# Kernel tuning notes

Hardware: AMD Instinct MI355X
Metric: run time of the kernel (lower is better)

Reference implementation:

```python
import jax, jax.numpy as jnp
import numpy as np

N, DIM = 100000, 512
HID = DIM // 2


def _mlp(z, W1, b1, W2, b2):
    # shared scorer: [N, dim] -> [N, 1]
    h = jax.nn.relu(z @ W1 + b1)
    return h @ W2 + b2


def setup_inputs() -> dict:
    key = jax.random.key(0)
    k1, k2, k3, k4 = jax.random.split(key, 4)
    s1 = 1.0 / np.sqrt(DIM)
    s2 = 1.0 / np.sqrt(HID)
    return {
        "z1": jax.random.normal(k1, (N, DIM), dtype=jnp.float32),
        "z2": jax.random.normal(k2, (N, DIM), dtype=jnp.float32),
        "W1": jax.random.normal(k3, (DIM, HID), dtype=jnp.float32) * s1,
        "b1": jnp.zeros((HID,), dtype=jnp.float32),
        "W2": jax.random.normal(k4, (HID, 1), dtype=jnp.float32) * s2,
        "b2": jnp.zeros((1,), dtype=jnp.float32),
    }


def reference(z1, z2, W1, b1, W2, b2):
    x = _mlp(z1, W1, b1, W2, b2)  # [N, 1]
    y = _mlp(z2, W1, b1, W2, b2)  # [N, 1]
    # exp-normalize pair: score_x = e^x / (e^x + e^y) == sigmoid(x - y)
    # computed exactly as in the original (plain exp, no max-subtract)
    e_x = jnp.exp(x)
    e_y = jnp.exp(y)
    denom = e_x + e_y
    score_x = e_x / denom  # [N, 1]
    score_y = e_y / denom  # [N, 1]
    # diag(score) @ z  ==  score * z  (row-wise broadcast scale)
    return score_x * z1 + score_y * z2
```

## Files before the change

kernel.cpp:

```cpp
#include <hip/hip_runtime.h>
#include <hip/hip_bf16.h>
#include <cmath>

#define DIM 512
#define HID 256
#define ROWS_PB 32
#define NCHUNK 16
#define CB 16384

typedef __attribute__((ext_vector_type(8))) short short8;
typedef __attribute__((ext_vector_type(4))) float f32x4;
typedef __attribute__((ext_vector_type(4))) unsigned int u32x4;

__device__ __forceinline__ unsigned short f2bf(float f) {
  union { float f; unsigned u; } v; v.f = f;
  unsigned u = v.u;
  return (unsigned short)((u + 0x7FFFu + ((u >> 16) & 1u)) >> 16);
}
__device__ __forceinline__ float bf2f(short h) {
  union { unsigned u; float f; } v;
  v.u = ((unsigned)(unsigned short)h) << 16;
  return v.f;
}

#define LGKM_BAR()                                        \
  do {                                                    \
    asm volatile("s_waitcnt lgkmcnt(0)" ::: "memory");    \
    __builtin_amdgcn_s_barrier();                         \
    __builtin_amdgcn_sched_barrier(0);                    \
  } while (0)

__global__ void w1_swz_kernel(const float* __restrict__ W1,
                              unsigned short* __restrict__ w1s) {
  int tid = blockIdx.x * blockDim.x + threadIdx.x;
  if (tid >= DIM * HID) return;
  int k = tid / HID;
  int c = tid - k * HID;
  w1s[(((k >> 3) * HID) + c) * 8 + (k & 7)] = f2bf(W1[tid]);
}

__device__ __forceinline__ short8 cvt8(const f32x4 p0, const f32x4 p1) {
  short8 r;
  r[0] = (short)f2bf(p0[0]); r[1] = (short)f2bf(p0[1]);
  r[2] = (short)f2bf(p0[2]); r[3] = (short)f2bf(p0[3]);
  r[4] = (short)f2bf(p1[0]); r[5] = (short)f2bf(p1[1]);
  r[6] = (short)f2bf(p1[2]); r[7] = (short)f2bf(p1[3]);
  return r;
}

__device__ __forceinline__ void wcombine(float wa, const short8 a, float wb,
                                         const short8 b, f32x4& o0, f32x4& o1) {
#pragma unroll
  for (int i = 0; i < 4; ++i) {
    o0[i] = wa * bf2f(a[i]) + wb * bf2f(b[i]);
    o1[i] = wa * bf2f(a[i + 4]) + wb * bf2f(b[i + 4]);
  }
}

__global__ __launch_bounds__(256, 2) void fa_main_kernel(
    const float* __restrict__ z1, const float* __restrict__ z2,
    const unsigned short* __restrict__ w1s,
    const float* __restrict__ bias1, const float* __restrict__ W2,
    const float* __restrict__ bias2, float* __restrict__ out, int n) {
  __shared__ char smem[81920];
  short8* Az = (short8*)smem;
  char* Bs = smem + 65536;
  float* xs = (float*)(smem + 65536);

  const int t = threadIdx.x;
  const int w = t >> 6;
  const int l = t & 63;
  const int l15 = l & 15, l16 = l >> 4;
  const int s = w & 1;
  const int tl = w >> 1;
  const int row0 = blockIdx.x * ROWS_PB;
  const int myrow = row0 + tl * 16 + l15;
  const bool rok = myrow < n;
  const float* zz = s ? z2 : z1;
  const float* ap = zz + (size_t)myrow * DIM + (l16 << 3);
  const f32x4 zf4 = (f32x4){0.f, 0.f, 0.f, 0.f};

  u32x4 breg0, breg1, breg2, breg3;
#define BLOAD(c)                                            \
  {                                                         \
    const u32x4* g = (const u32x4*)w1s + (c) * 1024 + t;    \
    breg0 = g[0];                                           \
    breg1 = g[256];                                         \
    breg2 = g[512];                                         \
    breg3 = g[768];                                         \
  }
#define BWRITE()                                            \
  {                                                         \
    u32x4* d = (u32x4*)Bs + t;                              \
    d[0] = breg0;                                           \
    d[256] = breg1;                                         \
    d[512] = breg2;                                         \
    d[768] = breg3;                                         \
  }

  BLOAD(0);
  f32x4 paA0, paA1, paB0, paB1;
  paA0 = rok ? *(const f32x4*)(ap) : zf4;
  paA1 = rok ? *(const f32x4*)(ap + 4) : zf4;
  paB0 = rok ? *(const f32x4*)(ap + 32) : zf4;
  paB1 = rok ? *(const f32x4*)(ap + 36) : zf4;
  BWRITE();
  __syncthreads();

  f32x4 acc[16];
#pragma unroll
  for (int f = 0; f < 16; ++f) acc[f] = zf4;

#pragma unroll
  for (int c = 0; c < NCHUNK; ++c) {
    if (c + 1 < NCHUNK) BLOAD(c + 1);
    short8 af;
    if (c & 1)
      af = cvt8(paB0, paB1);
    else
      af = cvt8(paA0, paA1);
    Az[((s * NCHUNK + c) * 2 + tl) * 64 + l] = af;
    if (c + 2 < NCHUNK) {
      const float* apn = ap + ((c + 2) << 5);
      if (c & 1) {
        paB0 = rok ? *(const f32x4*)(apn) : zf4;
        paB1 = rok ? *(const f32x4*)(apn + 4) : zf4;
      } else {
        paA0 = rok ? *(const f32x4*)(apn) : zf4;
        paA1 = rok ? *(const f32x4*)(apn + 4) : zf4;
      }
    }
    __builtin_amdgcn_sched_barrier(0);
    const short8* bp = (const short8*)Bs + (l16 << 8) + l15;
    short8 bf[16];
#pragma unroll
    for (int f = 0; f < 16; ++f) bf[f] = bp[f << 4];
    __builtin_amdgcn_sched_barrier(0);
#pragma unroll
    for (int f = 0; f < 16; ++f)
      acc[f] =
          __builtin_amdgcn_mfma_f32_16x16x32_bf16(af, bf[f], acc[f], 0, 0, 0);
    LGKM_BAR();
    if (c + 1 < NCHUNK) BWRITE();
    LGKM_BAR();
  }

  float part[4] = {0.f, 0.f, 0.f, 0.f};
#pragma unroll
  for (int f = 0; f < 16; ++f) {
    const int cc = (f << 4) + l15;
    const float w2v = W2[cc];
    const float b1v = bias1[cc];
#pragma unroll
    for (int r = 0; r < 4; ++r) {
      const float hh = acc[f][r] + b1v;
      part[r] += (hh > 0.f) ? hh * w2v : 0.f;
    }
  }
#pragma unroll
  for (int r = 0; r < 4; ++r) {
#pragma unroll
    for (int m = 1; m < 16; m <<= 1) part[r] += __shfl_xor(part[r], m, 16);
  }
  if (l15 == 0) {
#pragma unroll
    for (int r = 0; r < 4; ++r)
      xs[s * ROWS_PB + tl * 16 + (l16 << 2) + r] = part[r];
  }
  __syncthreads();

  const float x = xs[tl * 16 + l15];
  const float y = xs[ROWS_PB + tl * 16 + l15];
  const float sx = 1.f / (1.f + __expf(y - x));
  const float sy = 1.f - sx;
  float* orow = out + (size_t)myrow * DIM + (l16 << 3);
  if (rok) {
#pragma unroll
    for (int j = 0; j < 8; ++j) {
      const int cc = (s << 3) + j;
      const short8 a0 = Az[((0 * NCHUNK + cc) * 2 + tl) * 64 + l];
      const short8 a1 = Az[((1 * NCHUNK + cc) * 2 + tl) * 64 + l];
      f32x4 o0, o1;
      wcombine(sx, a0, sy, a1, o0, o1);
      *(f32x4*)(orow + (cc << 5)) = o0;
      *(f32x4*)(orow + (cc << 5) + 4) = o1;
    }
  }
#undef BLOAD
#undef BWRITE
}

extern "C" void kernel_launch(void* const* d_in, const int* in_sizes, int n_in,
                              void* d_out, int out_size, void* d_ws,
                              size_t ws_size, hipStream_t stream) {
  const float* z1 = (const float*)d_in[0];
  const float* z2 = (const float*)d_in[1];
  const float* W1 = (const float*)d_in[2];
  const float* b1 = (const float*)d_in[3];
  const float* W2 = (const float*)d_in[4];
  const float* b2 = (const float*)d_in[5];
  float* out = (float*)d_out;
  const int n = in_sizes[0] / DIM;
  unsigned short* w1s = (unsigned short*)d_ws;

  hipLaunchKernelGGL(w1_swz_kernel, dim3((DIM * HID + 255) / 256), dim3(256),
                     0, stream, W1, w1s);
  const int nwg = (n + ROWS_PB - 1) / ROWS_PB;
  hipLaunchKernelGGL(fa_main_kernel, dim3(nwg), dim3(256), 0, stream, z1, z2,
                     w1s, b1, W2, b2, out, n);
}
```

Before: 184.4 us.

## Make main kernel persistent and prefetch next tile during output epilogue

Launches a fixed grid of 512 workgroups that loop over row tiles in a grid-stride fashion instead of one workgroup per tile. Before writing the current tile's output, each workgroup issues the first W1 chunk and z-row loads for its next tile, so those loads overlap the output store phase. This aims to cut launch and ramp-up cost across about 3125 tiles and hide load latency between tiles. In exchange it adds an extra barrier per tile, keeps more registers live across the loop, and may leave the CUs unevenly loaded when the tile count does not divide evenly across workgroups.

```diff
diff --git a/kernel.cpp b/kernel.cpp
--- a/kernel.cpp
+++ b/kernel.cpp
@@ -6,7 +6,7 @@
 #define HID 256
 #define ROWS_PB 32
 #define NCHUNK 16
-#define CB 16384
+#define NBLK 512
 
 typedef __attribute__((ext_vector_type(8))) short short8;
 typedef __attribute__((ext_vector_type(4))) float f32x4;
@@ -73,12 +73,9 @@
   const int l15 = l & 15, l16 = l >> 4;
   const int s = w & 1;
   const int tl = w >> 1;
-  const int row0 = blockIdx.x * ROWS_PB;
-  const int myrow = row0 + tl * 16 + l15;
-  const bool rok = myrow < n;
   const float* zz = s ? z2 : z1;
-  const float* ap = zz + (size_t)myrow * DIM + (l16 << 3);
   const f32x4 zf4 = (f32x4){0.f, 0.f, 0.f, 0.f};
+  const int ntiles = (n + ROWS_PB - 1) / ROWS_PB;
 
   u32x4 breg0, breg1, breg2, breg3;
 #define BLOAD(c)                                            \
@@ -98,6 +95,13 @@
     d[768] = breg3;                                         \
   }
 
+  int tile = blockIdx.x;
+  if (tile >= ntiles) return;
+  int row0 = tile * ROWS_PB;
+  int myrow = row0 + tl * 16 + l15;
+  bool rok = myrow < n;
+  const float* ap = zz + (size_t)myrow * DIM + (l16 << 3);
+
   BLOAD(0);
   f32x4 paA0, paA1, paB0, paB1;
   paA0 = rok ? *(const f32x4*)(ap) : zf4;
@@ -107,84 +111,116 @@
   BWRITE();
   __syncthreads();
 
-  f32x4 acc[16];
-#pragma unroll
-  for (int f = 0; f < 16; ++f) acc[f] = zf4;
-
-#pragma unroll
-  for (int c = 0; c < NCHUNK; ++c) {
-    if (c + 1 < NCHUNK) BLOAD(c + 1);
-    short8 af;
-    if (c & 1)
-      af = cvt8(paB0, paB1);
-    else
-      af = cvt8(paA0, paA1);
-    Az[((s * NCHUNK + c) * 2 + tl) * 64 + l] = af;
-    if (c + 2 < NCHUNK) {
-      const float* apn = ap + ((c + 2) << 5);
-      if (c & 1) {
-        paB0 = rok ? *(const f32x4*)(apn) : zf4;
-        paB1 = rok ? *(const f32x4*)(apn + 4) : zf4;
-      } else {
-        paA0 = rok ? *(const f32x4*)(apn) : zf4;
-        paA1 = rok ? *(const f32x4*)(apn + 4) : zf4;
+  for (;;) {
+    f32x4 acc[16];
+#pragma unroll
+    for (int f = 0; f < 16; ++f) acc[f] = zf4;
+
+#pragma unroll
+    for (int c = 0; c < NCHUNK; ++c) {
+      if (c + 1 < NCHUNK) BLOAD(c + 1);
+      short8 af;
+      if (c & 1)
+        af = cvt8(paB0, paB1);
+      else
+        af = cvt8(paA0, paA1);
+      Az[((s * NCHUNK + c) * 2 + tl) * 64 + l] = af;
+      if (c + 2 < NCHUNK) {
+        const float* apn2 = ap + ((c + 2) << 5);
+        if (c & 1) {
+          paB0 = rok ? *(const f32x4*)(apn2) : zf4;
+          paB1 = rok ? *(const f32x4*)(apn2 + 4) : zf4;
+        } else {
+          paA0 = rok ? *(const f32x4*)(apn2) : zf4;
+          paA1 = rok ? *(const f32x4*)(apn2 + 4) : zf4;
+        }
       }
-    }
-    __builtin_amdgcn_sched_barrier(0);
-    const short8* bp = (const short8*)Bs + (l16 << 8) + l15;
-    short8 bf[16];
-#pragma unroll
-    for (int f = 0; f < 16; ++f) bf[f] = bp[f << 4];
-    __builtin_amdgcn_sched_barrier(0);
-#pragma unroll
-    for (int f = 0; f < 16; ++f)
-      acc[f] =
-          __builtin_amdgcn_mfma_f32_16x16x32_bf16(af, bf[f], acc[f], 0, 0, 0);
+      __builtin_amdgcn_sched_barrier(0);
+      const short8* bp = (const short8*)Bs + (l16 << 8) + l15;
+      short8 bf[16];
+#pragma unroll
+      for (int f = 0; f < 16; ++f) bf[f] = bp[f << 4];
+      __builtin_amdgcn_sched_barrier(0);
+#pragma unroll
+      for (int f = 0; f < 16; ++f)
+        acc[f] = __builtin_amdgcn_mfma_f32_16x16x32_bf16(af, bf[f], acc[f],
+                                                         0, 0, 0);
+      LGKM_BAR();
+      if (c + 1 < NCHUNK) BWRITE();
+      LGKM_BAR();
+    }
+
+    float part[4] = {0.f, 0.f, 0.f, 0.f};
+#pragma unroll
+    for (int f = 0; f < 16; ++f) {
+      const int cc = (f << 4) + l15;
+      const float w2v = W2[cc];
+      const float b1v = bias1[cc];
+#pragma unroll
+      for (int r = 0; r < 4; ++r) {
+        const float hh = acc[f][r] + b1v;
+        part[r] += (hh > 0.f) ? hh * w2v : 0.f;
+      }
+    }
+#pragma unroll
+    for (int r = 0; r < 4; ++r) {
+#pragma unroll
+      for (int m = 1; m < 16; m <<= 1) part[r] += __shfl_xor(part[r], m, 16);
+    }
+    if (l15 == 0) {
+#pragma unroll
+      for (int r = 0; r < 4; ++r)
+        xs[s * ROWS_PB + tl * 16 + (l16 << 2) + r] = part[r];
+    }
+    __syncthreads();
+
+    const int ntile = tile + NBLK;
+    const bool more = ntile < ntiles;
+    int nrow0 = 0, nmyrow = 0;
+    bool nrok = false;
+    const float* apn = zz;
+    if (more) {
+      nrow0 = ntile * ROWS_PB;
+      nmyrow = nrow0 + tl * 16 + l15;
+      nrok = nmyrow < n;
+      apn = zz + (size_t)nmyrow * DIM + (l16 << 3);
+      BLOAD(0);
+      paA0 = nrok ? *(const f32x4*)(apn) : zf4;
+      paA1 = nrok ? *(const f32x4*)(apn + 4) : zf4;
+      paB0 = nrok ? *(const f32x4*)(apn + 32) : zf4;
+      paB1 = nrok ? *(const f32x4*)(apn + 36) : zf4;
+      __builtin_amdgcn_sched_barrier(0);
+    }
+
+    {
+      const float x = xs[tl * 16 + l15];
+      const float y = xs[ROWS_PB + tl * 16 + l15];
+      const float sx = 1.f / (1.f + __expf(y - x));
+      const float sy = 1.f - sx;
+      float* orow = out + (size_t)myrow * DIM + (l16 << 3);
+      if (rok) {
+#pragma unroll
+        for (int j = 0; j < 8; ++j) {
+          const int cc = (s << 3) + j;
+          const short8 a0 = Az[((0 * NCHUNK + cc) * 2 + tl) * 64 + l];
+          const short8 a1 = Az[((1 * NCHUNK + cc) * 2 + tl) * 64 + l];
+          f32x4 o0, o1;
+          wcombine(sx, a0, sy, a1, o0, o1);
+          *(f32x4*)(orow + (cc << 5)) = o0;
+          *(f32x4*)(orow + (cc << 5) + 4) = o1;
+        }
+      }
+    }
+    __syncthreads();
+
+    if (!more) break;
+    BWRITE();
+    tile = ntile;
+    row0 = nrow0;
+    myrow = nmyrow;
+    rok = nrok;
+    ap = apn;
     LGKM_BAR();
-    if (c + 1 < NCHUNK) BWRITE();
-    LGKM_BAR();
-  }
-
-  float part[4] = {0.f, 0.f, 0.f, 0.f};
-#pragma unroll
-  for (int f = 0; f < 16; ++f) {
-    const int cc = (f << 4) + l15;
-    const float w2v = W2[cc];
-    const float b1v = bias1[cc];
-#pragma unroll
-    for (int r = 0; r < 4; ++r) {
-      const float hh = acc[f][r] + b1v;
-      part[r] += (hh > 0.f) ? hh * w2v : 0.f;
-    }
-  }
-#pragma unroll
-  for (int r = 0; r < 4; ++r) {
-#pragma unroll
-    for (int m = 1; m < 16; m <<= 1) part[r] += __shfl_xor(part[r], m, 16);
-  }
-  if (l15 == 0) {
-#pragma unroll
-    for (int r = 0; r < 4; ++r)
-      xs[s * ROWS_PB + tl * 16 + (l16 << 2) + r] = part[r];
-  }
-  __syncthreads();
-
-  const float x = xs[tl * 16 + l15];
-  const float y = xs[ROWS_PB + tl * 16 + l15];
-  const float sx = 1.f / (1.f + __expf(y - x));
-  const float sy = 1.f - sx;
-  float* orow = out + (size_t)myrow * DIM + (l16 << 3);
-  if (rok) {
-#pragma unroll
-    for (int j = 0; j < 8; ++j) {
-      const int cc = (s << 3) + j;
-      const short8 a0 = Az[((0 * NCHUNK + cc) * 2 + tl) * 64 + l];
-      const short8 a1 = Az[((1 * NCHUNK + cc) * 2 + tl) * 64 + l];
-      f32x4 o0, o1;
-      wcombine(sx, a0, sy, a1, o0, o1);
-      *(f32x4*)(orow + (cc << 5)) = o0;
-      *(f32x4*)(orow + (cc << 5) + 4) = o1;
-    }
   }
 #undef BLOAD
 #undef BWRITE
@@ -206,6 +242,7 @@
   hipLaunchKernelGGL(w1_swz_kernel, dim3((DIM * HID + 255) / 256), dim3(256),
                      0, stream, W1, w1s);
   const int nwg = (n + ROWS_PB - 1) / ROWS_PB;
-  hipLaunchKernelGGL(fa_main_kernel, dim3(nwg), dim3(256), 0, stream, z1, z2,
-                     w1s, b1, W2, b2, out, n);
-}
+  const int grid = nwg < NBLK ? nwg : NBLK;
+  hipLaunchKernelGGL(fa_main_kernel, dim3(grid), dim3(256), 0, stream, z1,
+                     z2, w1s, b1, W2, b2, out, n);
+}
```

Result: slower. 303.9 us (+64.8%).
